# Kernel tuning notes

Measured on AMD Instinct MI355X. Metric: run time of the kernel, lower is better.

## Reference

```python
import jax, jax.numpy as jnp
import numpy as np

N_NODES = 50000
N_EDGES = 1600000
C = 128
N_LAYERS = 8


def setup_inputs() -> dict:
    key = jax.random.key(0)
    ks = jax.random.split(key, 10)
    s = lambda fan_in: 1.0 / np.sqrt(fan_in)
    return {
        "x": jax.random.normal(ks[0], (N_NODES, C), dtype=jnp.float32),
        "edge_index": jax.random.randint(ks[1], (2, N_EDGES), 0, N_NODES, dtype=jnp.int32),
        "convs_W": jax.random.normal(ks[2], (N_LAYERS, C, C), dtype=jnp.float32) * s(C),
        "convs_b": jax.random.normal(ks[3], (N_LAYERS, C), dtype=jnp.float32) * s(C),
        "fc0_W": jax.random.normal(ks[4], (2 * C, C), dtype=jnp.float32) * s(2 * C),
        "fc0_b": jax.random.normal(ks[5], (C,), dtype=jnp.float32) * s(2 * C),
        "fc1_W": jax.random.normal(ks[6], (C, C), dtype=jnp.float32) * s(C),
        "fc1_b": jax.random.normal(ks[7], (C,), dtype=jnp.float32) * s(C),
        "fc2_W": jax.random.normal(ks[8], (C, 1), dtype=jnp.float32) * s(C),
        "fc2_b": jax.random.normal(ks[9], (1,), dtype=jnp.float32) * s(C),
    }


def reference(x, edge_index, convs_W, convs_b, fc0_W, fc0_b, fc1_W, fc1_b, fc2_W, fc2_b):
    N = x.shape[0]
    row, col = edge_index[0], edge_index[1]

    # GCNConv default: add self-loops, symmetric D^{-1/2}(A+I)D^{-1/2} normalization
    loops = jnp.arange(N, dtype=row.dtype)
    row_sl = jnp.concatenate([row, loops])  # source of message
    col_sl = jnp.concatenate([col, loops])  # target of aggregation
    deg = jax.ops.segment_sum(jnp.ones(row_sl.shape[0], x.dtype), col_sl, num_segments=N)
    dis = jnp.where(deg > 0, jax.lax.rsqrt(deg), 0.0)
    norm = dis[row_sl] * dis[col_sl]  # [E + N]

    def gcn_conv(h, W, b):
        h = h @ W                                  # [N, C]
        msg = h[row_sl] * norm[:, None]            # [E+N, C] gather + scale
        agg = jax.ops.segment_sum(msg, col_sl, num_segments=N)
        return agg + b

    h = jax.nn.relu(gcn_conv(x, convs_W[0], convs_b[0]))
    for i in range(1, convs_W.shape[0]):
        h = jax.nn.relu(gcn_conv(h, convs_W[i], convs_b[i]) + h)

    # edge MLP classifier on cat([h[src], h[dst]])
    e = jnp.concatenate([h[row], h[col]], axis=1)  # [E, 2C]
    e = jax.nn.relu(e @ fc0_W + fc0_b)
    e = jax.nn.relu(e @ fc1_W + fc1_b)
    return e @ fc2_W + fc2_b                       # [E, 1]
```

## Files before the change

kernel.cpp:

```cpp
#include <hip/hip_runtime.h>

#define C 128

typedef __attribute__((ext_vector_type(4))) float float4v;
typedef _Float16 half8v __attribute__((ext_vector_type(8)));
typedef _Float16 half4v __attribute__((ext_vector_type(4)));

__global__ void k_degree(const int* __restrict__ col, int* __restrict__ cnt, int E) {
  int e = blockIdx.x * blockDim.x + threadIdx.x;
  if (e < E) atomicAdd(&cnt[col[e]], 1);
}

__global__ void k_scan_part(const int* __restrict__ cnt, int* __restrict__ part,
                            int N) {
  __shared__ int sb[256];
  int t = threadIdx.x;
  int i = blockIdx.x * 256 + t;
  sb[t] = (i < N) ? cnt[i] : 0;
  __syncthreads();
#pragma unroll
  for (int off = 128; off > 0; off >>= 1) {
    if (t < off) sb[t] += sb[t + off];
    __syncthreads();
  }
  if (t == 0) part[blockIdx.x] = sb[0];
}

__global__ void k_scan_mid(int* __restrict__ part, int P) {
  __shared__ int sb[256];
  int t = threadIdx.x;
  int v = (t < P) ? part[t] : 0;
  sb[t] = v;
  __syncthreads();
#pragma unroll
  for (int off = 1; off < 256; off <<= 1) {
    int u = (t >= off) ? sb[t - off] : 0;
    __syncthreads();
    sb[t] += u;
    __syncthreads();
  }
  if (t < P) part[t] = sb[t] - v;
}

__global__ void k_scan_fin(const int* __restrict__ cnt, const int* __restrict__ part,
                           float* __restrict__ dis, int* __restrict__ indptr,
                           int* __restrict__ cursor, int N) {
  __shared__ int sb[256];
  int t = threadIdx.x;
  int i = blockIdx.x * 256 + t;
  int v = (i < N) ? cnt[i] : 0;
  sb[t] = v;
  __syncthreads();
#pragma unroll
  for (int off = 1; off < 256; off <<= 1) {
    int u = (t >= off) ? sb[t - off] : 0;
    __syncthreads();
    sb[t] += u;
    __syncthreads();
  }
  int run = part[blockIdx.x] + sb[t] - v;
  if (i < N) {
    indptr[i] = run;
    cursor[i] = run;
    dis[i] = rsqrtf((float)(v + 1));
    if (i == N - 1) indptr[N] = run + v;
  }
}

__global__ void k_csrfill(const int* __restrict__ row, const int* __restrict__ col,
                          const float* __restrict__ dis, int* __restrict__ cursor,
                          int2* __restrict__ emeta, int2* __restrict__ epair,
                          int* __restrict__ inv, int E) {
  int e = blockIdx.x * blockDim.x + threadIdx.x;
  if (e >= E) return;
  int r = row[e], c = col[e];
  int pos = atomicAdd(&cursor[c], 1);
  float nrm = dis[r] * dis[c];
  emeta[pos] = make_int2(r, __float_as_int(nrm));
  epair[pos] = make_int2(r, c);
  inv[e] = pos;
}

__global__ void k_cvt(const float* __restrict__ x, _Float16* __restrict__ xh, int n4) {
  int i = blockIdx.x * 256 + threadIdx.x;
  if (i >= n4) return;
  float4 v = ((const float4*)x)[i];
  half4v o = {(_Float16)v.x, (_Float16)v.y, (_Float16)v.z, (_Float16)v.w};
  *(half4v*)(xh + i * 4) = o;
}

__global__ void k_prepwf(const float* __restrict__ W1, _Float16* __restrict__ Wf) {
  int idx = blockIdx.x * 256 + threadIdx.x;
  int e = idx & 7, lane = (idx >> 3) & 63, j = (idx >> 9) & 7, kk = idx >> 12;
  int n = j * 16 + (lane & 15);
  int k = (kk * 4 + (lane >> 4)) * 8 + e;
  Wf[idx] = (_Float16)W1[k * C + n];
}

__global__ void k_prepw2(const float* __restrict__ convs_W,
                         const float* __restrict__ fc0_W,
                         _Float16* __restrict__ Wfh, _Float16* __restrict__ Wfl) {
  int g = blockIdx.x * 256 + threadIdx.x;
  int mat = g >> 14, idx = g & 16383;
  int e = idx & 7, lane = (idx >> 3) & 63, j = (idx >> 9) & 7, kk = idx >> 12;
  int n = j * 16 + (lane & 15);
  int k = (kk * 4 + (lane >> 4)) * 8 + e;
  const float* src = (mat < 8) ? convs_W + ((size_t)mat << 14)
                               : fc0_W + ((size_t)(mat - 8) << 14);
  float v = src[k * C + n];
  _Float16 h = (_Float16)v;
  Wfh[g] = h;
  Wfl[g] = (_Float16)((v - (float)h) * 4096.f);
}

__global__ __launch_bounds__(256)
void k_agg(const _Float16* __restrict__ h, const int* __restrict__ indptr,
           const int2* __restrict__ emeta, const float* __restrict__ dis,
           _Float16* __restrict__ agg, int N) {
  int w = (blockIdx.x * 256 + threadIdx.x) >> 6;
  int lane = threadIdx.x & 63;
  if (w >= N) return;
  int g16 = lane >> 4, c8 = lane & 15;
  int s = indptr[w], e = indptr[w + 1];
  float acc[8];
#pragma unroll
  for (int j = 0; j < 8; ++j) acc[j] = 0.f;

  int i = s;
  for (; i + 16 <= e; i += 16) {
    int2 m[4];
#pragma unroll
    for (int u = 0; u < 4; ++u) m[u] = emeta[i + u * 4 + g16];
    half8v hv[4];
#pragma unroll
    for (int u = 0; u < 4; ++u)
      hv[u] = *(const half8v*)(h + (size_t)m[u].x * C + c8 * 8);
#pragma unroll
    for (int u = 0; u < 4; ++u) {
      float nn = __int_as_float(m[u].y);
#pragma unroll
      for (int j = 0; j < 8; ++j) acc[j] += nn * (float)hv[u][j];
    }
  }
  for (; i + 4 <= e; i += 4) {
    int2 m = emeta[i + g16];
    half8v hv = *(const half8v*)(h + (size_t)m.x * C + c8 * 8);
    float nn = __int_as_float(m.y);
#pragma unroll
    for (int j = 0; j < 8; ++j) acc[j] += nn * (float)hv[j];
  }
  if (i < e) {
    int idx = i + g16;
    int2 m = make_int2(w, 0);
    if (idx < e) m = emeta[idx];
    half8v hv = *(const half8v*)(h + (size_t)m.x * C + c8 * 8);
    float nn = __int_as_float(m.y);
#pragma unroll
    for (int j = 0; j < 8; ++j) acc[j] += nn * (float)hv[j];
  }
#pragma unroll
  for (int j = 0; j < 8; ++j) {
    acc[j] += __shfl_xor(acc[j], 16, 64);
    acc[j] += __shfl_xor(acc[j], 32, 64);
  }
  if (lane < 16) {
    float dv = dis[w];
    float dv2 = dv * dv;
    half8v hs = *(const half8v*)(h + (size_t)w * C + lane * 8);
    half8v o;
#pragma unroll
    for (int j = 0; j < 8; ++j) o[j] = (_Float16)(acc[j] + dv2 * (float)hs[j]);
    *(half8v*)(agg + (size_t)w * C + lane * 8) = o;
  }
}

__global__ __launch_bounds__(256, 4)
void k_gemm_f16(const _Float16* __restrict__ A,
                const _Float16* __restrict__ Wfh, const _Float16* __restrict__ Wfl,
                const float* __restrict__ bias, const _Float16* __restrict__ skip,
                _Float16* __restrict__ out, int M, int relu) {
  int t = threadIdx.x;
  int r0 = blockIdx.x * 64;
  int w = t >> 6, lane = t & 63;
  int m0 = w * 16, lm = lane & 15, lq = lane >> 4;
  int row = r0 + m0 + lm;
  if (row >= M) row = M - 1;
  const _Float16* Ar = A + (size_t)row * C;

  float4v acch[8], accl[8];
#pragma unroll
  for (int j = 0; j < 8; ++j) {
    acch[j] = (float4v){0.f, 0.f, 0.f, 0.f};
    accl[j] = (float4v){0.f, 0.f, 0.f, 0.f};
  }
#pragma unroll
  for (int kk = 0; kk < 4; ++kk) {
    half8v a = *(const half8v*)(Ar + kk * 32 + lq * 8);
#pragma unroll
    for (int j = 0; j < 8; ++j) {
      int fi = ((kk * 8 + j) * 64 + lane) << 3;
      half8v bh = *(const half8v*)(Wfh + fi);
      half8v bl = *(const half8v*)(Wfl + fi);
      acch[j] = __builtin_amdgcn_mfma_f32_16x16x32_f16(a, bh, acch[j], 0, 0, 0);
      accl[j] = __builtin_amdgcn_mfma_f32_16x16x32_f16(a, bl, accl[j], 0, 0, 0);
    }
  }
#pragma unroll
  for (int j = 0; j < 8; ++j) {
    int n = j * 16 + lm;
    float bv = bias ? bias[n] : 0.f;
#pragma unroll
    for (int r = 0; r < 4; ++r) {
      int m = r0 + m0 + lq * 4 + r;
      if (m >= M) continue;
      float v = acch[j][r] + accl[j][r] * (1.f / 4096.f) + bv;
      if (skip) v += (float)skip[(size_t)m * C + n];
      if (relu) v = fmaxf(v, 0.f);
      out[(size_t)m * C + n] = (_Float16)v;
    }
  }
}

__global__ __launch_bounds__(256, 2)
void k_edge(const _Float16* __restrict__ P, const _Float16* __restrict__ Q,
            const int2* __restrict__ epair, const _Float16* __restrict__ Wf,
            const float* __restrict__ b1, const float* __restrict__ w2,
            const float* __restrict__ b2, float* __restrict__ tmpout, int E) {
  int t = threadIdx.x;
  int w = t >> 6, lane = t & 63;
  int lm = lane & 15, lq = lane >> 4;
  int base = blockIdx.x * 256 + w * 64;

  half8v a[4][4];
#pragma unroll
  for (int tt = 0; tt < 4; ++tt) {
    int p = base + tt * 16 + lm;
    int pc = (p < E) ? p : (E - 1);
    int2 rc = epair[pc];
    const _Float16* Pp = P + (size_t)rc.x * C + lq * 8;
    const _Float16* Qp = Q + (size_t)rc.y * C + lq * 8;
#pragma unroll
    for (int kk = 0; kk < 4; ++kk) {
      half8v pa = *(const half8v*)(Pp + kk * 32);
      half8v qa = *(const half8v*)(Qp + kk * 32);
      half8v s = pa + qa;
#pragma unroll
      for (int j = 0; j < 8; ++j)
        s[j] = (s[j] > (_Float16)0.f) ? s[j] : (_Float16)0.f;
      a[tt][kk] = s;
    }
  }

  float4v acc[4][8];
#pragma unroll
  for (int tt = 0; tt < 4; ++tt)
#pragma unroll
    for (int j = 0; j < 8; ++j) acc[tt][j] = (float4v){0.f, 0.f, 0.f, 0.f};

#pragma unroll
  for (int kk = 0; kk < 4; ++kk) {
#pragma unroll
    for (int j = 0; j < 8; ++j) {
      half8v b = *(const half8v*)(Wf + (((kk * 8 + j) * 64 + lane) << 3));
#pragma unroll
      for (int tt = 0; tt < 4; ++tt)
        acc[tt][j] = __builtin_amdgcn_mfma_f32_16x16x32_f16(a[tt][kk], b,
                                                            acc[tt][j], 0, 0, 0);
    }
  }

  float b1v[8], w2v[8];
#pragma unroll
  for (int j = 0; j < 8; ++j) {
    int n = j * 16 + lm;
    b1v[j] = b1[n];
    w2v[j] = w2[n];
  }
  float bb = b2[0];
#pragma unroll
  for (int tt = 0; tt < 4; ++tt) {
    float partv[4] = {0.f, 0.f, 0.f, 0.f};
#pragma unroll
    for (int j = 0; j < 8; ++j) {
#pragma unroll
      for (int r = 0; r < 4; ++r) {
        float e2 = fmaxf(acc[tt][j][r] + b1v[j], 0.f);
        partv[r] = fmaf(e2, w2v[j], partv[r]);
      }
    }
#pragma unroll
    for (int off = 1; off < 16; off <<= 1) {
#pragma unroll
      for (int r = 0; r < 4; ++r) partv[r] += __shfl_xor(partv[r], off, 64);
    }
    if (lm == 0) {
#pragma unroll
      for (int r = 0; r < 4; ++r) {
        int pe = base + tt * 16 + lq * 4 + r;
        if (pe < E) tmpout[pe] = partv[r] + bb;
      }
    }
  }
}

__global__ void k_perm(const float* __restrict__ tmp, const int* __restrict__ inv,
                       float* __restrict__ out, int E) {
  int e = blockIdx.x * 256 + threadIdx.x;
  if (e < E) out[e] = tmp[inv[e]];
}

extern "C" void kernel_launch(void* const* d_in, const int* in_sizes, int n_in,
                              void* d_out, int out_size, void* d_ws, size_t ws_size,
                              hipStream_t stream) {
  const float* x       = (const float*)d_in[0];
  const int*   ei      = (const int*)d_in[1];
  const float* convs_W = (const float*)d_in[2];
  const float* convs_b = (const float*)d_in[3];
  const float* fc0_W   = (const float*)d_in[4];
  const float* fc0_b   = (const float*)d_in[5];
  const float* fc1_W   = (const float*)d_in[6];
  const float* fc1_b   = (const float*)d_in[7];
  const float* fc2_W   = (const float*)d_in[8];
  const float* fc2_b   = (const float*)d_in[9];
  float* out = (float*)d_out;

  const int N = in_sizes[0] / C;
  const int E = in_sizes[1] / 2;
  const int L = in_sizes[2] / (C * C);
  const int* row = ei;
  const int* col = ei + E;
  const int SB = (N + 255) / 256;

  char* wp = (char*)d_ws;
  auto carve = [&](size_t bytes) {
    char* p = wp; wp += (bytes + 255) & ~(size_t)255; return p;
  };
  int*      cnt    = (int*)carve((size_t)N * 4);
  int*      part   = (int*)carve((size_t)SB * 4);
  int*      indptr = (int*)carve((size_t)(N + 1) * 4);
  int*      cursor = (int*)carve((size_t)N * 4);
  float*    dis    = (float*)carve((size_t)N * 4);
  int2*     emeta  = (int2*)carve((size_t)E * 8);
  int2*     epair  = (int2*)carve((size_t)E * 8);
  int*      inv    = (int*)carve((size_t)E * 4);
  float*    tmpout = (float*)carve((size_t)E * 4);
  _Float16* Wf     = (_Float16*)carve((size_t)C * C * 2);
  _Float16* Wfh    = (_Float16*)carve((size_t)10 * C * C * 2);
  _Float16* Wfl    = (_Float16*)carve((size_t)10 * C * C * 2);
  _Float16* xh     = (_Float16*)carve((size_t)N * C * 2);
  _Float16* h0     = (_Float16*)carve((size_t)N * C * 2);
  _Float16* h1     = (_Float16*)carve((size_t)N * C * 2);
  _Float16* aggb   = (_Float16*)carve((size_t)N * C * 2);
  _Float16* Pm     = (_Float16*)carve((size_t)N * C * 2);
  _Float16* Qm     = (_Float16*)carve((size_t)N * C * 2);

  hipMemsetAsync(cnt, 0, (size_t)N * 4, stream);
  k_degree<<<(E + 255) / 256, 256, 0, stream>>>(col, cnt, E);
  k_scan_part<<<SB, 256, 0, stream>>>(cnt, part, N);
  k_scan_mid<<<1, 256, 0, stream>>>(part, SB);
  k_scan_fin<<<SB, 256, 0, stream>>>(cnt, part, dis, indptr, cursor, N);
  k_csrfill<<<(E + 255) / 256, 256, 0, stream>>>(row, col, dis, cursor,
                                                 emeta, epair, inv, E);
  k_prepwf<<<C * C / 256, 256, 0, stream>>>(fc1_W, Wf);
  k_prepw2<<<10 * C * C / 256, 256, 0, stream>>>(convs_W, fc0_W, Wfh, Wfl);
  k_cvt<<<(N * C / 4 + 255) / 256, 256, 0, stream>>>(x, xh, N * C / 4);

  int aggBlocks  = (N * 64 + 255) / 256;
  int gemmBlocks = (N + 63) / 64;
  const int MSZ = C * C;

  k_agg<<<aggBlocks, 256, 0, stream>>>(xh, indptr, emeta, dis, aggb, N);
  k_gemm_f16<<<gemmBlocks, 256, 0, stream>>>(aggb, Wfh, Wfl, convs_b,
                                             nullptr, h0, N, 1);
  _Float16* hcur = h0; _Float16* hoth = h1;
  for (int l = 1; l < L; ++l) {
    k_agg<<<aggBlocks, 256, 0, stream>>>(hcur, indptr, emeta, dis, aggb, N);
    k_gemm_f16<<<gemmBlocks, 256, 0, stream>>>(aggb, Wfh + (size_t)l * MSZ,
                                               Wfl + (size_t)l * MSZ,
                                               convs_b + (size_t)l * C, hcur,
                                               hoth, N, 1);
    _Float16* tmp = hcur; hcur = hoth; hoth = tmp;
  }
  k_gemm_f16<<<gemmBlocks, 256, 0, stream>>>(hcur, Wfh + (size_t)8 * MSZ,
                                             Wfl + (size_t)8 * MSZ, nullptr,
                                             nullptr, Pm, N, 0);
  k_gemm_f16<<<gemmBlocks, 256, 0, stream>>>(hcur, Wfh + (size_t)9 * MSZ,
                                             Wfl + (size_t)9 * MSZ, fc0_b,
                                             nullptr, Qm, N, 0);
  k_edge<<<(E + 255) / 256, 256, 0, stream>>>(Pm, Qm, epair, Wf, fc1_b,
                                              fc2_W, fc2_b, tmpout, E);
  k_perm<<<(E + 255) / 256, 256, 0, stream>>>(tmpout, inv, out, E);
}
```

Measured before the change: 1.085 ms.

## Prefetch edge metadata in aggregation, stage edge-MLP weights in LDS, add nontemporal accesses

In the aggregation kernel, the next chunk of edge metadata is loaded one iteration ahead with nontemporal loads, and the self-loop feature and degree loads are hoisted to the start. The edge kernel now copies the fc1 weight fragments into shared memory per block and processes 32 edges per wave instead of 64, which halves the accumulators so occupancy can rise to 4 blocks per CU. Streamed edge indices, outputs and the permutation use nontemporal loads and stores to avoid polluting the caches. In exchange, each edge block repeats a 32KB weight copy into LDS and there are twice as many blocks.

Measured after the change: 1.060 ms. 2.3% less time.

```diff
diff --git a/kernel.cpp b/kernel.cpp
--- a/kernel.cpp
+++ b/kernel.cpp
@@ -122,39 +122,72 @@
   if (w >= N) return;
   int g16 = lane >> 4, c8 = lane & 15;
   int s = indptr[w], e = indptr[w + 1];
+
+  float dv = 0.f;
+  half8v hs = {};
+  if (lane < 16) {
+    dv = dis[w];
+    hs = *(const half8v*)(h + (size_t)w * C + lane * 8);
+  }
+
   float acc[8];
 #pragma unroll
   for (int j = 0; j < 8; ++j) acc[j] = 0.f;
 
   int i = s;
-  for (; i + 16 <= e; i += 16) {
-    int2 m[4];
-#pragma unroll
-    for (int u = 0; u < 4; ++u) m[u] = emeta[i + u * 4 + g16];
+  long long mc[4];
+  if (i + 16 <= e) {
+#pragma unroll
+    for (int u = 0; u < 4; ++u)
+      mc[u] = __builtin_nontemporal_load(
+          (const long long*)&emeta[i + u * 4 + g16]);
+  }
+  for (; i + 16 <= e;) {
+    int inext = i + 16;
+    bool hn = (inext + 16 <= e);
+    long long mn[4];
+    if (hn) {
+#pragma unroll
+      for (int u = 0; u < 4; ++u)
+        mn[u] = __builtin_nontemporal_load(
+            (const long long*)&emeta[inext + u * 4 + g16]);
+    }
     half8v hv[4];
 #pragma unroll
-    for (int u = 0; u < 4; ++u)
-      hv[u] = *(const half8v*)(h + (size_t)m[u].x * C + c8 * 8);
-#pragma unroll
     for (int u = 0; u < 4; ++u) {
-      float nn = __int_as_float(m[u].y);
+      int srcn = (int)(mc[u] & 0xffffffffLL);
+      hv[u] = *(const half8v*)(h + (size_t)srcn * C + c8 * 8);
+    }
+#pragma unroll
+    for (int u = 0; u < 4; ++u) {
+      float nn = __int_as_float((int)(mc[u] >> 32));
 #pragma unroll
       for (int j = 0; j < 8; ++j) acc[j] += nn * (float)hv[u][j];
     }
+    if (hn) {
+#pragma unroll
+      for (int u = 0; u < 4; ++u) mc[u] = mn[u];
+    }
+    i = inext;
   }
   for (; i + 4 <= e; i += 4) {
-    int2 m = emeta[i + g16];
-    half8v hv = *(const half8v*)(h + (size_t)m.x * C + c8 * 8);
-    float nn = __int_as_float(m.y);
+    long long m = __builtin_nontemporal_load((const long long*)&emeta[i + g16]);
+    int srcn = (int)(m & 0xffffffffLL);
+    half8v hv = *(const half8v*)(h + (size_t)srcn * C + c8 * 8);
+    float nn = __int_as_float((int)(m >> 32));
 #pragma unroll
     for (int j = 0; j < 8; ++j) acc[j] += nn * (float)hv[j];
   }
   if (i < e) {
     int idx = i + g16;
-    int2 m = make_int2(w, 0);
-    if (idx < e) m = emeta[idx];
-    half8v hv = *(const half8v*)(h + (size_t)m.x * C + c8 * 8);
-    float nn = __int_as_float(m.y);
+    int srcn = w;
+    float nn = 0.f;
+    if (idx < e) {
+      long long m = __builtin_nontemporal_load((const long long*)&emeta[idx]);
+      srcn = (int)(m & 0xffffffffLL);
+      nn = __int_as_float((int)(m >> 32));
+    }
+    half8v hv = *(const half8v*)(h + (size_t)srcn * C + c8 * 8);
 #pragma unroll
     for (int j = 0; j < 8; ++j) acc[j] += nn * (float)hv[j];
   }
@@ -164,9 +197,7 @@
     acc[j] += __shfl_xor(acc[j], 32, 64);
   }
   if (lane < 16) {
-    float dv = dis[w];
     float dv2 = dv * dv;
-    half8v hs = *(const half8v*)(h + (size_t)w * C + lane * 8);
     half8v o;
 #pragma unroll
     for (int j = 0; j < 8; ++j) o[j] = (_Float16)(acc[j] + dv2 * (float)hs[j]);
@@ -221,24 +252,33 @@
   }
 }
 
-__global__ __launch_bounds__(256, 2)
+__global__ __launch_bounds__(256, 4)
 void k_edge(const _Float16* __restrict__ P, const _Float16* __restrict__ Q,
             const int2* __restrict__ epair, const _Float16* __restrict__ Wf,
             const float* __restrict__ b1, const float* __restrict__ w2,
             const float* __restrict__ b2, float* __restrict__ tmpout, int E) {
+  __shared__ __align__(16) _Float16 WL[16384];
   int t = threadIdx.x;
+#pragma unroll
+  for (int it = 0; it < 8; ++it) {
+    int off = it * 2048 + t * 8;
+    *(half8v*)(WL + off) = *(const half8v*)(Wf + off);
+  }
+
   int w = t >> 6, lane = t & 63;
   int lm = lane & 15, lq = lane >> 4;
-  int base = blockIdx.x * 256 + w * 64;
-
-  half8v a[4][4];
-#pragma unroll
-  for (int tt = 0; tt < 4; ++tt) {
+  int base = blockIdx.x * 128 + w * 32;
+
+  half8v a[2][4];
+#pragma unroll
+  for (int tt = 0; tt < 2; ++tt) {
     int p = base + tt * 16 + lm;
     int pc = (p < E) ? p : (E - 1);
-    int2 rc = epair[pc];
-    const _Float16* Pp = P + (size_t)rc.x * C + lq * 8;
-    const _Float16* Qp = Q + (size_t)rc.y * C + lq * 8;
+    long long ev = __builtin_nontemporal_load((const long long*)&epair[pc]);
+    int rx = (int)(ev & 0xffffffffLL);
+    int ry = (int)(ev >> 32);
+    const _Float16* Pp = P + (size_t)rx * C + lq * 8;
+    const _Float16* Qp = Q + (size_t)ry * C + lq * 8;
 #pragma unroll
     for (int kk = 0; kk < 4; ++kk) {
       half8v pa = *(const half8v*)(Pp + kk * 32);
@@ -250,10 +290,11 @@
       a[tt][kk] = s;
     }
   }
-
-  float4v acc[4][8];
-#pragma unroll
-  for (int tt = 0; tt < 4; ++tt)
+  __syncthreads();
+
+  float4v acc[2][8];
+#pragma unroll
+  for (int tt = 0; tt < 2; ++tt)
 #pragma unroll
     for (int j = 0; j < 8; ++j) acc[tt][j] = (float4v){0.f, 0.f, 0.f, 0.f};
 
@@ -261,9 +302,9 @@
   for (int kk = 0; kk < 4; ++kk) {
 #pragma unroll
     for (int j = 0; j < 8; ++j) {
-      half8v b = *(const half8v*)(Wf + (((kk * 8 + j) * 64 + lane) << 3));
-#pragma unroll
-      for (int tt = 0; tt < 4; ++tt)
+      half8v b = *(const half8v*)(WL + (((kk * 8 + j) * 64 + lane) << 3));
+#pragma unroll
+      for (int tt = 0; tt < 2; ++tt)
         acc[tt][j] = __builtin_amdgcn_mfma_f32_16x16x32_f16(a[tt][kk], b,
                                                             acc[tt][j], 0, 0, 0);
     }
@@ -278,7 +319,7 @@
   }
   float bb = b2[0];
 #pragma unroll
-  for (int tt = 0; tt < 4; ++tt) {
+  for (int tt = 0; tt < 2; ++tt) {
     float partv[4] = {0.f, 0.f, 0.f, 0.f};
 #pragma unroll
     for (int j = 0; j < 8; ++j) {
@@ -297,7 +338,7 @@
 #pragma unroll
       for (int r = 0; r < 4; ++r) {
         int pe = base + tt * 16 + lq * 4 + r;
-        if (pe < E) tmpout[pe] = partv[r] + bb;
+        if (pe < E) __builtin_nontemporal_store(partv[r] + bb, &tmpout[pe]);
       }
     }
   }
@@ -306,7 +347,11 @@
 __global__ void k_perm(const float* __restrict__ tmp, const int* __restrict__ inv,
                        float* __restrict__ out, int E) {
   int e = blockIdx.x * 256 + threadIdx.x;
-  if (e < E) out[e] = tmp[inv[e]];
+  if (e < E) {
+    int idx = __builtin_nontemporal_load(&inv[e]);
+    float v = __builtin_nontemporal_load(&tmp[idx]);
+    __builtin_nontemporal_store(v, &out[e]);
+  }
 }
 
 extern "C" void kernel_launch(void* const* d_in, const int* in_sizes, int n_in,
@@ -387,7 +432,7 @@
   k_gemm_f16<<<gemmBlocks, 256, 0, stream>>>(hcur, Wfh + (size_t)9 * MSZ,
                                              Wfl + (size_t)9 * MSZ, fc0_b,
                                              nullptr, Qm, N, 0);
-  k_edge<<<(E + 255) / 256, 256, 0, stream>>>(Pm, Qm, epair, Wf, fc1_b,
+  k_edge<<<(E + 127) / 128, 256, 0, stream>>>(Pm, Qm, epair, Wf, fc1_b,
                                               fc2_W, fc2_b, tmpout, E);
   k_perm<<<(E + 255) / 256, 256, 0, stream>>>(tmpout, inv, out, E);
 }
```
